# Optimization experiments

Hardware: AMD Instinct MI355X
Metric: run time of the kernel (lower is better)

Reference implementation:

```python
import jax, jax.numpy as jnp
import numpy as np

A = 5          # num anchors
C = 80         # num classes
STRIDE = 16    # network stride
THRESH = 0.6
OBJ_SCALE = 5.0
NOOBJ_SCALE = 1.0
COORD_SCALE = 1.0
CLASS_SCALE = 1.0


def setup_inputs() -> dict:
    key = jax.random.key(0)
    k1, k2, k3, k4 = jax.random.split(key, 4)
    B, H, W, N = 16, 64, 64, 50
    output = jax.random.normal(k1, (B, A * (5 + C), H, W), dtype=jnp.float32)
    cls_id = jax.random.randint(k2, (B, N, 1), 0, C).astype(jnp.float32)
    cxcy = jax.random.uniform(k3, (B, N, 2), dtype=jnp.float32) * (W * STRIDE)
    wh = jax.random.uniform(k4, (B, N, 2), dtype=jnp.float32) * 290.0 + 10.0
    target = jnp.concatenate([cls_id, cxcy, wh], axis=-1)  # (B, N, 5)
    anchors = jnp.array([[18.3, 21.6], [60.0, 66.0], [106.8, 175.5],
                         [252.2, 112.9], [312.7, 293.4]], dtype=jnp.float32)
    return {"output": output, "target": target, "anchors": anchors}


def _iou(g, p):
    # g: (B, N, 4), p: (B, M, 4), boxes in [cx, cy, w, h]
    gx1, gy1 = g[..., 0] - g[..., 2] / 2, g[..., 1] - g[..., 3] / 2
    gx2, gy2 = g[..., 0] + g[..., 2] / 2, g[..., 1] + g[..., 3] / 2
    px1, py1 = p[..., 0] - p[..., 2] / 2, p[..., 1] - p[..., 3] / 2
    px2, py2 = p[..., 0] + p[..., 2] / 2, p[..., 1] + p[..., 3] / 2
    ix1 = jnp.maximum(gx1[:, :, None], px1[:, None, :])
    iy1 = jnp.maximum(gy1[:, :, None], py1[:, None, :])
    ix2 = jnp.minimum(gx2[:, :, None], px2[:, None, :])
    iy2 = jnp.minimum(gy2[:, :, None], py2[:, None, :])
    inter = jnp.clip(ix2 - ix1, 0) * jnp.clip(iy2 - iy1, 0)
    g_area = (gx2 - gx1) * (gy2 - gy1)
    p_area = (px2 - px1) * (py2 - py1)
    union = g_area[:, :, None] + p_area[:, None, :] - inter + 1e-6
    return inter / union  # (B, N, M)


def reference(output, target, anchors):
    B, _, H, W = output.shape
    out = output.reshape(B, A, 5 + C, H, W).transpose(0, 1, 3, 4, 2)  # (B,A,H,W,5+C)
    coord = out[..., :4]
    conf = out[..., 4]
    cls_logits = out[..., 5:]

    gx = jnp.arange(W, dtype=output.dtype)
    gy = jnp.arange(H, dtype=output.dtype)
    px = (jax.nn.sigmoid(coord[..., 0]) + gx[None, None, None, :]) * STRIDE
    py = (jax.nn.sigmoid(coord[..., 1]) + gy[None, None, :, None]) * STRIDE
    pw = jnp.exp(coord[..., 2]) * anchors[:, 0][None, :, None, None]
    ph = jnp.exp(coord[..., 3]) * anchors[:, 1][None, :, None, None]
    pred_boxes = jnp.stack([px, py, pw, ph], axis=-1).reshape(B, -1, 4)  # (B, A*H*W, 4)

    gt_boxes = target[..., 1:]  # (B, N, 4)
    gt_cls = target[..., 0]     # (B, N)

    iou = _iou(gt_boxes, pred_boxes)          # (B, N, M)
    best_iou = iou.max(axis=1)                # (B, M)
    best_idx = iou.argmax(axis=1)             # (B, M)

    mask = (best_iou > THRESH).reshape(B, A, H, W)
    mask_f = mask.astype(output.dtype)
    conf_mask = jnp.where(mask, OBJ_SCALE, NOOBJ_SCALE).astype(output.dtype)

    tcoord = jnp.take_along_axis(gt_boxes, best_idx[..., None], axis=1)  # (B, M, 4)
    tcoord = tcoord.reshape(B, A, H, W, 4) * mask_f[..., None]
    tcls = jnp.take_along_axis(gt_cls, best_idx, axis=1).reshape(B, A, H, W)
    tcls_idx = (tcls * mask_f).astype(jnp.int32)
    tconf = mask_f

    cm = mask_f[..., None]
    coord_loss = COORD_SCALE * jnp.sum((coord * cm - tcoord * cm) ** 2)
    conf_loss = jnp.sum((conf * conf_mask - tconf * conf_mask) ** 2)
    logp = jax.nn.log_softmax(cls_logits, axis=-1)
    nll = -jnp.take_along_axis(logp, tcls_idx[..., None], axis=-1)[..., 0]
    cls_loss = CLASS_SCALE * jnp.sum(jnp.where(mask, nll, 0.0))

    return coord_loss + conf_loss + cls_loss
```

## Files before the change

kernel.cpp:

```cpp
#include <hip/hip_runtime.h>

#define A_   5
#define C_   80
#define BB   16
#define HH   64
#define WW   64
#define NN   50
#define CH   (5 + C_)
#define HW   (HH * WW)
#define STRIDE_F 16.0f
#define THRESH_F 0.6f

__global__ void zero_out_kernel(float* out) { out[0] = 0.0f; }

__global__ __launch_bounds__(256)
void region_loss_kernel(const float* __restrict__ out4d,
                        const float* __restrict__ target,
                        const float* __restrict__ anchors,
                        float* __restrict__ loss)
{
    __shared__ float g_x1[NN], g_y1[NN], g_x2[NN], g_y2[NN], g_area[NN];
    __shared__ float g_cx[NN], g_cy[NN], g_w[NN], g_h[NN], g_cls[NN];
    __shared__ float wave_sum[4];

    const int bid = blockIdx.x;
    const int h4  = bid & 15;
    const int a   = (bid >> 4) % A_;
    const int b   = bid / (A_ * 16);

    const int tid = threadIdx.x;
    const int w   = tid & 63;
    const int h   = (h4 << 2) + (tid >> 6);

    if (tid < NN) {
        const float* t = target + ((size_t)b * NN + tid) * 5;
        float cls = t[0], cx = t[1], cy = t[2], gw = t[3], gh = t[4];
        g_cls[tid]  = cls;
        g_cx[tid]   = cx;  g_cy[tid] = cy;  g_w[tid] = gw;  g_h[tid] = gh;
        g_x1[tid]   = cx - gw * 0.5f;  g_y1[tid] = cy - gh * 0.5f;
        g_x2[tid]   = cx + gw * 0.5f;  g_y2[tid] = cy + gh * 0.5f;
        g_area[tid] = gw * gh;
    }
    __syncthreads();

    const float* base = out4d + (size_t)(b * (A_ * CH) + a * CH) * HW + h * WW + w;

    const float x0 = base[0 * HW];
    const float x1 = base[1 * HW];
    const float x2 = base[2 * HW];
    const float x3 = base[3 * HW];
    const float cf = base[4 * HW];

    const float aw = anchors[a * 2 + 0];
    const float ah = anchors[a * 2 + 1];

    const float px = (1.0f / (1.0f + __expf(-x0)) + (float)w) * STRIDE_F;
    const float py = (1.0f / (1.0f + __expf(-x1)) + (float)h) * STRIDE_F;
    const float pw = __expf(x2) * aw;
    const float ph = __expf(x3) * ah;
    const float px1 = px - pw * 0.5f, py1 = py - ph * 0.5f;
    const float px2 = px + pw * 0.5f, py2 = py + ph * 0.5f;
    const float parea = pw * ph;

    float best_inter = 0.0f, best_union = 1.0f;
    int best_n = 0;
    for (int n = 0; n < NN; ++n) {
        float ix1 = fmaxf(g_x1[n], px1);
        float iy1 = fmaxf(g_y1[n], py1);
        float ix2 = fminf(g_x2[n], px2);
        float iy2 = fminf(g_y2[n], py2);
        float iw  = fmaxf(ix2 - ix1, 0.0f);
        float ih  = fmaxf(iy2 - iy1, 0.0f);
        float inter = iw * ih;
        float uni   = g_area[n] + parea - inter + 1e-6f;
        if (inter * best_union > best_inter * uni) {
            best_inter = inter; best_union = uni; best_n = n;
        }
    }
    const bool mask = best_inter > THRESH_F * best_union;

    float local;
    if (mask) {
        float d0 = x0 - g_cx[best_n];
        float d1 = x1 - g_cy[best_n];
        float d2 = x2 - g_w[best_n];
        float d3 = x3 - g_h[best_n];
        float cd = 5.0f * cf - 5.0f;
        local = d0*d0 + d1*d1 + d2*d2 + d3*d3 + cd*cd;
    } else {
        local = cf * cf;
    }

    const unsigned long long any_mask = __ballot(mask);
    if (any_mask != 0ull) {
        const int tcls = mask ? (int)g_cls[best_n] : 0;
        float m = -1e30f, s = 0.0f, xt = 0.0f;
        #pragma unroll 4
        for (int c = 0; c < C_; ++c) {
            float x  = base[(5 + c) * HW];
            float nm = fmaxf(m, x);
            s = s * __expf(m - nm) + __expf(x - nm);
            m = nm;
            if (c == tcls) xt = x;
        }
        float lse = m + __logf(s);
        if (mask) local += lse - xt;
    }

    for (int off = 32; off > 0; off >>= 1)
        local += __shfl_down(local, off);
    if ((tid & 63) == 0) wave_sum[tid >> 6] = local;
    __syncthreads();
    if (tid == 0)
        atomicAdd(loss, wave_sum[0] + wave_sum[1] + wave_sum[2] + wave_sum[3]);
}

extern "C" void kernel_launch(void* const* d_in, const int* in_sizes, int n_in,
                              void* d_out, int out_size, void* d_ws, size_t ws_size,
                              hipStream_t stream) {
    const float* output  = (const float*)d_in[0];
    const float* target  = (const float*)d_in[1];
    const float* anchors = (const float*)d_in[2];
    float* loss = (float*)d_out;

    zero_out_kernel<<<1, 1, 0, stream>>>(loss);

    const int grid = BB * A_ * (HH / 4);
    region_loss_kernel<<<grid, 256, 0, stream>>>(output, target, anchors, loss);
}
```

Measured before the change: 164.1 us.

## Precompute GT boxes in prep kernel and use two-pass softmax for masked cells

The zero-init kernel becomes a prep kernel that precomputes ground-truth corner boxes and areas into global device arrays. The main kernel reads these as float4 instead of building a shared-memory copy per block, which removes a __syncthreads and redundant setup work. The class log-sum-exp moves to a two-pass max-then-sum-of-exp with multiple accumulators, and only masked lanes run it rather than the whole wave when any lane is masked. This breaks the serial dependency of the online softmax but reads the class logits twice and makes the loop divergent within a wave.

```diff
diff --git a/kernel.cpp b/kernel.cpp
--- a/kernel.cpp
+++ b/kernel.cpp
@@ -9,9 +9,22 @@
 #define CH   (5 + C_)
 #define HW   (HH * WW)
 #define STRIDE_F 16.0f
-#define THRESH_F 0.6f
 
-__global__ void zero_out_kernel(float* out) { out[0] = 0.0f; }
+__device__ __align__(16) float4 g_box[BB * NN];
+__device__ float g_area[BB * NN];
+
+__global__ void prep_kernel(const float* __restrict__ target, float* __restrict__ loss)
+{
+    const int i = blockIdx.x * blockDim.x + threadIdx.x;
+    if (i == 0) loss[0] = 0.0f;
+    if (i < BB * NN) {
+        const float* t = target + (size_t)i * 5;
+        const float cx = t[1], cy = t[2], w = t[3], h = t[4];
+        g_box[i]  = make_float4(cx - 0.5f * w, cy - 0.5f * h,
+                                cx + 0.5f * w, cy + 0.5f * h);
+        g_area[i] = w * h + 1e-6f;
+    }
+}
 
 __global__ __launch_bounds__(256)
 void region_loss_kernel(const float* __restrict__ out4d,
@@ -19,8 +32,6 @@
                         const float* __restrict__ anchors,
                         float* __restrict__ loss)
 {
-    __shared__ float g_x1[NN], g_y1[NN], g_x2[NN], g_y2[NN], g_area[NN];
-    __shared__ float g_cx[NN], g_cy[NN], g_w[NN], g_h[NN], g_cls[NN];
     __shared__ float wave_sum[4];
 
     const int bid = blockIdx.x;
@@ -31,17 +42,6 @@
     const int tid = threadIdx.x;
     const int w   = tid & 63;
     const int h   = (h4 << 2) + (tid >> 6);
-
-    if (tid < NN) {
-        const float* t = target + ((size_t)b * NN + tid) * 5;
-        float cls = t[0], cx = t[1], cy = t[2], gw = t[3], gh = t[4];
-        g_cls[tid]  = cls;
-        g_cx[tid]   = cx;  g_cy[tid] = cy;  g_w[tid] = gw;  g_h[tid] = gh;
-        g_x1[tid]   = cx - gw * 0.5f;  g_y1[tid] = cy - gh * 0.5f;
-        g_x2[tid]   = cx + gw * 0.5f;  g_y2[tid] = cy + gh * 0.5f;
-        g_area[tid] = gw * gh;
-    }
-    __syncthreads();
 
     const float* base = out4d + (size_t)(b * (A_ * CH) + a * CH) * HW + h * WW + w;
 
@@ -62,49 +62,58 @@
     const float px2 = px + pw * 0.5f, py2 = py + ph * 0.5f;
     const float parea = pw * ph;
 
+    const float4* __restrict__ box = g_box  + b * NN;
+    const float*  __restrict__ ar  = g_area + b * NN;
+
     float best_inter = 0.0f, best_union = 1.0f;
     int best_n = 0;
+    #pragma unroll 10
     for (int n = 0; n < NN; ++n) {
-        float ix1 = fmaxf(g_x1[n], px1);
-        float iy1 = fmaxf(g_y1[n], py1);
-        float ix2 = fminf(g_x2[n], px2);
-        float iy2 = fminf(g_y2[n], py2);
+        const float4 g  = box[n];
+        const float  ga = ar[n];
+        float ix1 = fmaxf(g.x, px1);
+        float iy1 = fmaxf(g.y, py1);
+        float ix2 = fminf(g.z, px2);
+        float iy2 = fminf(g.w, py2);
         float iw  = fmaxf(ix2 - ix1, 0.0f);
         float ih  = fmaxf(iy2 - iy1, 0.0f);
         float inter = iw * ih;
-        float uni   = g_area[n] + parea - inter + 1e-6f;
+        float uni   = (ga + parea) - inter;
         if (inter * best_union > best_inter * uni) {
             best_inter = inter; best_union = uni; best_n = n;
         }
     }
-    const bool mask = best_inter > THRESH_F * best_union;
+    const bool mask = best_inter > 0.6f * best_union;
 
-    float local;
+    float local = cf * cf;
     if (mask) {
-        float d0 = x0 - g_cx[best_n];
-        float d1 = x1 - g_cy[best_n];
-        float d2 = x2 - g_w[best_n];
-        float d3 = x3 - g_h[best_n];
-        float cd = 5.0f * cf - 5.0f;
-        local = d0*d0 + d1*d1 + d2*d2 + d3*d3 + cd*cd;
-    } else {
-        local = cf * cf;
-    }
+        const float* t = target + ((size_t)(b * NN + best_n)) * 5;
+        const float d0 = x0 - t[1];
+        const float d1 = x1 - t[2];
+        const float d2 = x2 - t[3];
+        const float d3 = x3 - t[4];
+        const float cd = 5.0f * cf - 5.0f;
 
-    const unsigned long long any_mask = __ballot(mask);
-    if (any_mask != 0ull) {
-        const int tcls = mask ? (int)g_cls[best_n] : 0;
-        float m = -1e30f, s = 0.0f, xt = 0.0f;
-        #pragma unroll 4
-        for (int c = 0; c < C_; ++c) {
-            float x  = base[(5 + c) * HW];
-            float nm = fmaxf(m, x);
-            s = s * __expf(m - nm) + __expf(x - nm);
-            m = nm;
-            if (c == tcls) xt = x;
+        float m0 = -1e30f, m1 = -1e30f, m2 = -1e30f, m3 = -1e30f;
+        #pragma unroll 5
+        for (int c = 0; c < C_; c += 4) {
+            m0 = fmaxf(m0, base[(5 + c) * HW]);
+            m1 = fmaxf(m1, base[(6 + c) * HW]);
+            m2 = fmaxf(m2, base[(7 + c) * HW]);
+            m3 = fmaxf(m3, base[(8 + c) * HW]);
         }
-        float lse = m + __logf(s);
-        if (mask) local += lse - xt;
+        const float m = fmaxf(fmaxf(m0, m1), fmaxf(m2, m3));
+
+        float s0 = 0.0f, s1 = 0.0f;
+        #pragma unroll 10
+        for (int c = 0; c < C_; c += 2) {
+            s0 += __expf(base[(5 + c) * HW] - m);
+            s1 += __expf(base[(6 + c) * HW] - m);
+        }
+        const int   tcls = (int)t[0];
+        const float xt   = base[(5 + tcls) * HW];
+        local = d0*d0 + d1*d1 + d2*d2 + d3*d3 + cd*cd
+              + (m + __logf(s0 + s1) - xt);
     }
 
     for (int off = 32; off > 0; off >>= 1)
@@ -123,7 +132,7 @@
     const float* anchors = (const float*)d_in[2];
     float* loss = (float*)d_out;
 
-    zero_out_kernel<<<1, 1, 0, stream>>>(loss);
+    prep_kernel<<<(BB * NN + 255) / 256, 256, 0, stream>>>(target, loss);
 
     const int grid = BB * A_ * (HH / 4);
     region_loss_kernel<<<grid, 256, 0, stream>>>(output, target, anchors, loss);
```

Result: no change. 162.2 us (-1.1%).
